# Kernel optimization log

Hardware: AMD Instinct MI355X
Metric: run time of the kernel (lower is better)

## Reference

```python
import jax, jax.numpy as jnp
import numpy as np

# Stickbreaking attention (IBM ModuleFormer style) as in the torch module:
#   logits = q @ k^T / sqrt(head_dim)  (causal)
#   z = sigmoid(logits), log_beta = logsigmoid(-logits), both causally masked
#   re_cum_log_beta = einsum('bhij,jk->bhik', log_beta, tril(ones(S,S)))
#     -> re[i,k] = sum_{k <= j <= i} log_beta[i, j]   (full tril incl. diagonal,
#        exactly as written in the source: cum_weight = torch.tril(torch.ones(L,L)))
#   weights = z * exp(re_cum_log_beta);  out = weights @ v
# Note: the torch code applies the causal mask by adding -inf; the only finite,
# NaN-free expression of that math (matching ModuleFormer's masked_fill) is to
# zero out masked entries of z and log_beta before the triangular matmul.

B, H, S, D = 2, 16, 1024, 64


def setup_inputs() -> dict:
    key = jax.random.key(0)
    kq, kk, kv = jax.random.split(key, 3)
    q = jax.random.normal(kq, (B, H, S, D), dtype=jnp.float32)
    k = jax.random.normal(kk, (B, H, S, D), dtype=jnp.float32)
    v = jax.random.normal(kv, (B, H, S, D), dtype=jnp.float32)
    return {"q": q, "k": k, "v": v}


def reference(q, k, v):
    head_dim = q.shape[-1]
    scaling = 1.0 / np.sqrt(head_dim).astype(np.float32)
    # [B,H,S,S] attention logits
    logits = jnp.einsum("bhqd,bhkd->bhqk", q, k) * scaling
    seq = logits.shape[-1]
    causal = jnp.tril(jnp.ones((seq, seq), dtype=logits.dtype))  # 1 where j<=i
    z = jax.nn.sigmoid(logits) * causal
    log_beta = jax.nn.log_sigmoid(-logits) * causal
    cum_weight = jnp.tril(jnp.ones((seq, seq), dtype=logits.dtype))
    # re[i,k] = sum_{j>=k} log_beta[i,j] (log_beta already 0 for j>i)
    re_cum_log_beta = jnp.einsum("bhij,jk->bhik", log_beta, cum_weight)
    weights = z * jnp.exp(re_cum_log_beta)
    return jnp.einsum("bhqk,bhkd->bhqd", weights, v)
```

## Files before the change

kernel.cpp:

```cpp
#include <hip/hip_runtime.h>
#include <hip/hip_bf16.h>
#include <math.h>


typedef __attribute__((ext_vector_type(8))) short short8;
typedef __attribute__((ext_vector_type(4))) short short4v;
typedef __attribute__((ext_vector_type(4))) float f32x4;

#define WPITCH 72
#define BLOB_SH 12288

__device__ inline short bf16r(float x) {
    __hip_bfloat16 h = __float2bfloat16(x);
    return *(short*)&h;
}
__device__ inline float bf16f(short s) {
    union { unsigned u; float f; } c;
    c.u = ((unsigned)(unsigned short)s) << 16;
    return c.f;
}

__global__ __launch_bounds__(256) void stickbreak_prep(
    const float* __restrict__ Kg, const float* __restrict__ Vg,
    short* __restrict__ ws)
{
    const int t = threadIdx.x;
    const int n = blockIdx.x;
    const float* kp = Kg + (size_t)n * 4096;
    const float* vp = Vg + (size_t)n * 4096;
    short* blob = ws + (size_t)n * BLOB_SH;

    const int lane = t & 63;
    const int l16 = lane & 15;
    const int q4 = lane >> 4;
    const int s0 = t >> 6;

    #pragma unroll
    for (int w = 0; w < 2; ++w) {
        const int s  = s0 + 4 * w;
        const int nt = s >> 1;
        const int ks = s & 1;
        {
            const float* src = kp + (16 * nt + l16) * 64 + 32 * ks + 8 * q4;
            const float4 f0 = *(const float4*)src;
            const float4 f1 = *(const float4*)(src + 4);
            float a[8] = {f0.x, f0.y, f0.z, f0.w, f1.x, f1.y, f1.z, f1.w};
            short8 h, l;
            #pragma unroll
            for (int e = 0; e < 8; ++e) {
                h[e] = bf16r(a[e]);
                l[e] = bf16r(a[e] - bf16f(h[e]));
            }
            *(short8*)&blob[s * 512 + lane * 8]        = h;
            *(short8*)&blob[4096 + s * 512 + lane * 8] = l;
        }
        {
            const float* vsrc = vp + (32 * ks + 8 * q4) * 64 + 16 * nt + l16;
            short8 wv8;
            #pragma unroll
            for (int e = 0; e < 8; ++e) wv8[e] = bf16r(vsrc[e * 64]);
            *(short8*)&blob[8192 + s * 512 + lane * 8] = wv8;
        }
    }
}

__global__ __launch_bounds__(256, 2) void stickbreak_main(
    const float* __restrict__ Qg, const short* __restrict__ ws,
    float* __restrict__ Og)
{
    __shared__ __align__(16) short Ws[64 * WPITCH];

    const int t = threadIdx.x;
    const int n = blockIdx.x;
    const int bh = (n & 7) + 8 * (n >> 7);
    const int qr = (n >> 3) & 15;
    const int qt = (n >> 8) ? (15 - qr) : qr;

    const size_t hbase = (size_t)bh * 1024 * 64;
    const float* qp = Qg + hbase + (size_t)qt * 64 * 64;
    const short* blobs = ws + (size_t)bh * 16 * BLOB_SH;
    float*       op = Og + hbase + (size_t)qt * 64 * 64;

    const int lane = t & 63;
    const int wv   = t >> 6;
    const int l16  = lane & 15;
    const int q4   = lane >> 4;

    short8 qfh[2], qfl[2];
    {
        const float* qrow = qp + (16 * wv + l16) * 64;
        #pragma unroll
        for (int ks = 0; ks < 2; ++ks) {
            const int base = 32 * ks + 8 * q4;
            const float4 f0 = *(const float4*)(qrow + base);
            const float4 f1 = *(const float4*)(qrow + base + 4);
            float a[8] = {f0.x, f0.y, f0.z, f0.w, f1.x, f1.y, f1.z, f1.w};
            #pragma unroll
            for (int j = 0; j < 8; ++j) {
                const short hi = bf16r(a[j]);
                qfh[ks][j] = hi;
                qfl[ks][j] = bf16r(a[j] - bf16f(hi));
            }
        }
    }

    f32x4 Oacc[4];
    #pragma unroll
    for (int i = 0; i < 4; ++i) Oacc[i] = (f32x4){0.f, 0.f, 0.f, 0.f};
    float Crow = 0.f;

    for (int kt = qt; kt >= 0; --kt) {
        const short* blob = blobs + (size_t)kt * BLOB_SH;

        short8 kh[8], kl[8], vb[8];
        #pragma unroll
        for (int s = 0; s < 8; ++s) {
            kh[s] = *(const short8*)&blob[s * 512 + lane * 8];
            kl[s] = *(const short8*)&blob[4096 + s * 512 + lane * 8];
        }
        #pragma unroll
        for (int s = 0; s < 8; ++s)
            vb[s] = *(const short8*)&blob[8192 + s * 512 + lane * 8];

        f32x4 Sacc[4];
        #pragma unroll
        for (int i = 0; i < 4; ++i) Sacc[i] = (f32x4){0.f, 0.f, 0.f, 0.f};
        #pragma unroll
        for (int ks = 0; ks < 2; ++ks) {
            #pragma unroll
            for (int nt = 0; nt < 4; ++nt) {
                const int s = nt * 2 + ks;
                Sacc[nt] = __builtin_amdgcn_mfma_f32_16x16x32_bf16(kh[s], qfh[ks], Sacc[nt], 0, 0, 0);
                Sacc[nt] = __builtin_amdgcn_mfma_f32_16x16x32_bf16(kl[s], qfh[ks], Sacc[nt], 0, 0, 0);
                Sacc[nt] = __builtin_amdgcn_mfma_f32_16x16x32_bf16(kh[s], qfl[ks], Sacc[nt], 0, 0, 0);
            }
        }

        const bool diag = (kt == qt);
        const int irow = 16 * wv + l16;
        float ex[4][4];
        float sR[4];
        #pragma unroll
        for (int nt = 0; nt < 4; ++nt) {
            float lbr[4], lv[4];
            #pragma unroll
            for (int reg = 0; reg < 4; ++reg) {
                float l = Sacc[nt][reg] * 0.125f;
                if (diag && (16 * nt + 4 * q4 + reg > irow)) l = -1e30f;
                const float e  = __expf(-fabsf(l));
                const float lb = -(fmaxf(l, 0.f) + __logf(1.f + e));
                lv[reg] = l; lbr[reg] = lb;
            }
            const float s3 = lbr[3];
            const float s2 = lbr[2] + s3;
            const float s1 = lbr[1] + s2;
            const float s0 = lbr[0] + s1;
            ex[nt][0] = lv[0] + lbr[0] + s0;
            ex[nt][1] = lv[1] + lbr[1] + s1;
            ex[nt][2] = lv[2] + lbr[2] + s2;
            ex[nt][3] = lv[3] + lbr[3] + s3;
            sR[nt] = s0;
        }
        float gq[4], Tn[4];
        #pragma unroll
        for (int nt = 0; nt < 4; ++nt) {
            float g = sR[nt];
            float u = __shfl_down(g, 16, 64); if (q4 < 3) g += u;
            u = __shfl_down(g, 32, 64);       if (q4 < 2) g += u;
            gq[nt] = g;
            Tn[nt] = __shfl(g, l16, 64);
        }
        const float TSa[4] = { Tn[1] + Tn[2] + Tn[3], Tn[2] + Tn[3], Tn[3], 0.f };
        #pragma unroll
        for (int nt = 0; nt < 4; ++nt) {
            const float cross = (gq[nt] - sR[nt]) + TSa[nt] + Crow;
            short4v w4;
            #pragma unroll
            for (int reg = 0; reg < 4; ++reg)
                w4[reg] = bf16r(__expf(ex[nt][reg] + cross));
            *(short4v*)&Ws[irow * WPITCH + 16 * nt + 4 * q4] = w4;
        }
        Crow += TSa[0] + Tn[0];

        #pragma unroll
        for (int ks = 0; ks < 2; ++ks) {
            const short8 wa = *(const short8*)&Ws[(16 * wv + l16) * WPITCH + 32 * ks + 8 * q4];
            #pragma unroll
            for (int dt = 0; dt < 4; ++dt) {
                Oacc[dt] = __builtin_amdgcn_mfma_f32_16x16x32_bf16(wa, vb[dt * 2 + ks], Oacc[dt], 0, 0, 0);
            }
        }
    }

    #pragma unroll
    for (int dt = 0; dt < 4; ++dt)
        #pragma unroll
        for (int r = 0; r < 4; ++r)
            op[(16 * wv + 4 * q4 + r) * 64 + 16 * dt + l16] = Oacc[dt][r];
}

extern "C" void kernel_launch(void* const* d_in, const int* in_sizes, int n_in,
                              void* d_out, int out_size, void* d_ws, size_t ws_size,
                              hipStream_t stream) {
    const float* q = (const float*)d_in[0];
    const float* k = (const float*)d_in[1];
    const float* v = (const float*)d_in[2];
    float* out = (float*)d_out;
    short* ws = (short*)d_ws;
    stickbreak_prep<<<dim3(512), dim3(256), 0, stream>>>(k, v, ws);
    stickbreak_main<<<dim3(512), dim3(256), 0, stream>>>(q, ws, out);
}
```

Before: 109.5 us.

## Split key range across two blocks per query tile and merge partial outputs

```diff
diff --git a/kernel.cpp b/kernel.cpp
--- a/kernel.cpp
+++ b/kernel.cpp
@@ -9,6 +9,8 @@
 
 #define WPITCH 72
 #define BLOB_SH 12288
+#define NBLOB 512
+#define VP 66
 
 __device__ inline short bf16r(float x) {
     __hip_bfloat16 h = __float2bfloat16(x);
@@ -24,6 +26,8 @@
     const float* __restrict__ Kg, const float* __restrict__ Vg,
     short* __restrict__ ws)
 {
+    __shared__ float Vlds[64 * VP];
+
     const int t = threadIdx.x;
     const int n = blockIdx.x;
     const float* kp = Kg + (size_t)n * 4096;
@@ -35,51 +39,75 @@
     const int q4 = lane >> 4;
     const int s0 = t >> 6;
 
+    {
+        const int row = t >> 2;
+        const int cb = (t & 3) << 4;
+        #pragma unroll
+        for (int c = 0; c < 4; ++c) {
+            const float4 f = *(const float4*)(vp + row * 64 + cb + 4 * c);
+            *(float2*)&Vlds[row * VP + cb + 4 * c]     = make_float2(f.x, f.y);
+            *(float2*)&Vlds[row * VP + cb + 4 * c + 2] = make_float2(f.z, f.w);
+        }
+    }
+
     #pragma unroll
     for (int w = 0; w < 2; ++w) {
         const int s  = s0 + 4 * w;
         const int nt = s >> 1;
         const int ks = s & 1;
-        {
-            const float* src = kp + (16 * nt + l16) * 64 + 32 * ks + 8 * q4;
-            const float4 f0 = *(const float4*)src;
-            const float4 f1 = *(const float4*)(src + 4);
-            float a[8] = {f0.x, f0.y, f0.z, f0.w, f1.x, f1.y, f1.z, f1.w};
-            short8 h, l;
-            #pragma unroll
-            for (int e = 0; e < 8; ++e) {
-                h[e] = bf16r(a[e]);
-                l[e] = bf16r(a[e] - bf16f(h[e]));
-            }
-            *(short8*)&blob[s * 512 + lane * 8]        = h;
-            *(short8*)&blob[4096 + s * 512 + lane * 8] = l;
-        }
-        {
-            const float* vsrc = vp + (32 * ks + 8 * q4) * 64 + 16 * nt + l16;
-            short8 wv8;
-            #pragma unroll
-            for (int e = 0; e < 8; ++e) wv8[e] = bf16r(vsrc[e * 64]);
-            *(short8*)&blob[8192 + s * 512 + lane * 8] = wv8;
-        }
-    }
-}
-
-__global__ __launch_bounds__(256, 2) void stickbreak_main(
+        const float* src = kp + (16 * nt + l16) * 64 + 32 * ks + 8 * q4;
+        const float4 f0 = *(const float4*)src;
+        const float4 f1 = *(const float4*)(src + 4);
+        float a[8] = {f0.x, f0.y, f0.z, f0.w, f1.x, f1.y, f1.z, f1.w};
+        short8 h, l;
+        #pragma unroll
+        for (int e = 0; e < 8; ++e) {
+            h[e] = bf16r(a[e]);
+            l[e] = bf16r(a[e] - bf16f(h[e]));
+        }
+        *(short8*)&blob[s * 512 + lane * 8]        = h;
+        *(short8*)&blob[4096 + s * 512 + lane * 8] = l;
+    }
+
+    __syncthreads();
+
+    #pragma unroll
+    for (int w = 0; w < 2; ++w) {
+        const int s  = s0 + 4 * w;
+        const int nt = s >> 1;
+        const int ks = s & 1;
+        const int d  = 16 * nt + l16;
+        const int jb = 32 * ks + 8 * q4;
+        short8 wv8;
+        #pragma unroll
+        for (int e = 0; e < 8; ++e) wv8[e] = bf16r(Vlds[(jb + e) * VP + d]);
+        *(short8*)&blob[8192 + s * 512 + lane * 8] = wv8;
+    }
+}
+
+__global__ __launch_bounds__(256, 4) void stickbreak_main(
     const float* __restrict__ Qg, const short* __restrict__ ws,
-    float* __restrict__ Og)
+    float* __restrict__ part)
 {
     __shared__ __align__(16) short Ws[64 * WPITCH];
 
     const int t = threadIdx.x;
     const int n = blockIdx.x;
-    const int bh = (n & 7) + 8 * (n >> 7);
-    const int qr = (n >> 3) & 15;
-    const int qt = (n >> 8) ? (15 - qr) : qr;
+    const int half = n >> 9;
+    const int m = n & 511;
+    const int bh = (m & 7) + 8 * (m >> 7);
+    const int qr = (m >> 3) & 15;
+    const int qt = (m >> 8) ? (15 - qr) : qr;
+    const int nl = (qt + 1) >> 1;
+    const int kstart = half ? (nl - 1) : qt;
+    const int kend   = half ? 0 : nl;
 
     const size_t hbase = (size_t)bh * 1024 * 64;
     const float* qp = Qg + hbase + (size_t)qt * 64 * 64;
     const short* blobs = ws + (size_t)bh * 16 * BLOB_SH;
-    float*       op = Og + hbase + (size_t)qt * 64 * 64;
+    const int g = bh * 16 + qt;
+    float* opart = part + (size_t)g * 8192 + (half ? 4096 : 0);
+    float* Cb = part + (size_t)NBLOB * 8192;
 
     const int lane = t & 63;
     const int wv   = t >> 6;
@@ -109,34 +137,35 @@
     for (int i = 0; i < 4; ++i) Oacc[i] = (f32x4){0.f, 0.f, 0.f, 0.f};
     float Crow = 0.f;
 
-    for (int kt = qt; kt >= 0; --kt) {
+    for (int kt = kstart; kt >= kend; --kt) {
         const short* blob = blobs + (size_t)kt * BLOB_SH;
 
-        short8 kh[8], kl[8], vb[8];
-        #pragma unroll
-        for (int s = 0; s < 8; ++s) {
-            kh[s] = *(const short8*)&blob[s * 512 + lane * 8];
-            kl[s] = *(const short8*)&blob[4096 + s * 512 + lane * 8];
-        }
+        f32x4 Sacc[4];
+        #pragma unroll
+        for (int i = 0; i < 4; ++i) Sacc[i] = (f32x4){0.f, 0.f, 0.f, 0.f};
+        #pragma unroll
+        for (int ks = 0; ks < 2; ++ks) {
+            short8 kh[4], kl[4];
+            #pragma unroll
+            for (int nt = 0; nt < 4; ++nt) {
+                const int s = nt * 2 + ks;
+                kh[nt] = *(const short8*)&blob[s * 512 + lane * 8];
+                kl[nt] = *(const short8*)&blob[4096 + s * 512 + lane * 8];
+            }
+            #pragma unroll
+            for (int nt = 0; nt < 4; ++nt) {
+                Sacc[nt] = __builtin_amdgcn_mfma_f32_16x16x32_bf16(kh[nt], qfh[ks], Sacc[nt], 0, 0, 0);
+                Sacc[nt] = __builtin_amdgcn_mfma_f32_16x16x32_bf16(kl[nt], qfh[ks], Sacc[nt], 0, 0, 0);
+                Sacc[nt] = __builtin_amdgcn_mfma_f32_16x16x32_bf16(kh[nt], qfl[ks], Sacc[nt], 0, 0, 0);
+            }
+        }
+
+        short8 vb[8];
         #pragma unroll
         for (int s = 0; s < 8; ++s)
             vb[s] = *(const short8*)&blob[8192 + s * 512 + lane * 8];
 
-        f32x4 Sacc[4];
-        #pragma unroll
-        for (int i = 0; i < 4; ++i) Sacc[i] = (f32x4){0.f, 0.f, 0.f, 0.f};
-        #pragma unroll
-        for (int ks = 0; ks < 2; ++ks) {
-            #pragma unroll
-            for (int nt = 0; nt < 4; ++nt) {
-                const int s = nt * 2 + ks;
-                Sacc[nt] = __builtin_amdgcn_mfma_f32_16x16x32_bf16(kh[s], qfh[ks], Sacc[nt], 0, 0, 0);
-                Sacc[nt] = __builtin_amdgcn_mfma_f32_16x16x32_bf16(kl[s], qfh[ks], Sacc[nt], 0, 0, 0);
-                Sacc[nt] = __builtin_amdgcn_mfma_f32_16x16x32_bf16(kh[s], qfl[ks], Sacc[nt], 0, 0, 0);
-            }
-        }
-
-        const bool diag = (kt == qt);
+        const bool diag = (half == 0) && (kt == qt);
         const int irow = 16 * wv + l16;
         float ex[4][4];
         float sR[4];
@@ -164,11 +193,11 @@
         float gq[4], Tn[4];
         #pragma unroll
         for (int nt = 0; nt < 4; ++nt) {
-            float g = sR[nt];
-            float u = __shfl_down(g, 16, 64); if (q4 < 3) g += u;
-            u = __shfl_down(g, 32, 64);       if (q4 < 2) g += u;
-            gq[nt] = g;
-            Tn[nt] = __shfl(g, l16, 64);
+            float g2 = sR[nt];
+            float u = __shfl_down(g2, 16, 64); if (q4 < 3) g2 += u;
+            u = __shfl_down(g2, 32, 64);       if (q4 < 2) g2 += u;
+            gq[nt] = g2;
+            Tn[nt] = __shfl(g2, l16, 64);
         }
         const float TSa[4] = { Tn[1] + Tn[2] + Tn[3], Tn[2] + Tn[3], Tn[3], 0.f };
         #pragma unroll
@@ -196,7 +225,33 @@
     for (int dt = 0; dt < 4; ++dt)
         #pragma unroll
         for (int r = 0; r < 4; ++r)
-            op[(16 * wv + 4 * q4 + r) * 64 + 16 * dt + l16] = Oacc[dt][r];
+            opart[(16 * wv + 4 * q4 + r) * 64 + 16 * dt + l16] = Oacc[dt][r];
+    if (half == 0 && q4 == 0)
+        Cb[(size_t)g * 64 + 16 * wv + l16] = Crow;
+}
+
+__global__ __launch_bounds__(256) void stickbreak_merge(
+    const float* __restrict__ part, float* __restrict__ out)
+{
+    const int g = blockIdx.x;
+    const int t = threadIdx.x;
+    const int i = t >> 2;
+    const int c0 = (t & 3) << 4;
+    const float* Ohi = part + (size_t)g * 8192 + i * 64 + c0;
+    const float* Olo = Ohi + 4096;
+    const float e = __expf(part[(size_t)NBLOB * 8192 + (size_t)g * 64 + i]);
+    float* o = out + (size_t)g * 4096 + i * 64 + c0;
+    #pragma unroll
+    for (int c = 0; c < 4; ++c) {
+        const float4 a = ((const float4*)Ohi)[c];
+        const float4 b = ((const float4*)Olo)[c];
+        float4 r;
+        r.x = fmaf(e, b.x, a.x);
+        r.y = fmaf(e, b.y, a.y);
+        r.z = fmaf(e, b.z, a.z);
+        r.w = fmaf(e, b.w, a.w);
+        ((float4*)o)[c] = r;
+    }
 }
 
 extern "C" void kernel_launch(void* const* d_in, const int* in_sizes, int n_in,
@@ -207,6 +262,8 @@
     const float* v = (const float*)d_in[2];
     float* out = (float*)d_out;
     short* ws = (short*)d_ws;
+    float* part = (float*)(ws + (size_t)NBLOB * BLOB_SH);
     stickbreak_prep<<<dim3(512), dim3(256), 0, stream>>>(k, v, ws);
-    stickbreak_main<<<dim3(512), dim3(256), 0, stream>>>(q, ws, out);
-}
+    stickbreak_main<<<dim3(1024), dim3(256), 0, stream>>>(q, ws, part);
+    stickbreak_merge<<<dim3(512), dim3(256), 0, stream>>>(part, out);
+}
```

Measured after the change: 107.6 us. About the same (-1.8%).
